# Kernel optimization log

Hardware: AMD Instinct MI355X
Metric: run time of the kernel (lower is better)

The kernel has to match this reference:

```python
import jax, jax.numpy as jnp
import numpy as np


def get_con_vecs(seq):
    # Faithful to torch: reshape (B,H,S,d) -> (B,S,H*d) (a raw reshape, as in the
    # original), right-pad along the sequence axis to length 2S with zeros, then
    # for each query position j, roll the padded sequence by (S - j).
    # Instead of a python loop of rolls over a repeated (B,S,2S,D) buffer, we
    # compute the roll as a single gather with precomputed indices.
    B, H, S, d = seq.shape
    D = H * d
    x = seq.reshape(B, S, D)
    padded = jnp.concatenate([x, jnp.zeros_like(x)], axis=1)  # (B, 2S, D)
    t = jnp.arange(2 * S)
    j = jnp.arange(S)
    # torch.roll(v, shift)[t] == v[(t - shift) mod N]; shift = S - j
    idx = (t[None, :] - (S - j[:, None])) % (2 * S)  # (S, 2S)
    new = padded[:, idx, :]  # (B, S, 2S, D)
    return new.reshape(B, H, S, 2 * S, d)


def setup_inputs() -> dict:
    key = jax.random.key(0)
    kq, kk, kv = jax.random.split(key, 3)
    B, H, S, d = 2, 8, 256, 64
    Q = jax.random.normal(kq, (B, H, S, d), dtype=jnp.float32)
    K = jax.random.normal(kk, (B, H, S, d), dtype=jnp.float32)
    V = jax.random.normal(kv, (B, H, S, d), dtype=jnp.float32)
    return {"Q": Q, "K": K, "V": V}


def reference(Q, K, V):
    # attn_type == 'con' branch of ScaledDotProductAttention.forward
    Q_c = get_con_vecs(Q)              # (B,H,S,2S,d)
    V_c = get_con_vecs(V)              # (B,H,S,2S,d)
    scores = jnp.sum(Q_c * V_c, axis=3)  # (B,H,S,d)
    attn = jax.nn.softmax(scores, axis=-1)
    context = attn * V                 # elementwise, (B,H,S,d)
    return (context, attn)
```

## Files before the change

### kernel.cpp

```cpp
#include <hip/hip_runtime.h>
#include <hip/hip_bf16.h>

#define B_ 2
#define H_ 8
#define S_ 256
#define D_ 64
#define PER_B (H_ * S_ * D_)
#define OUT_HALF (B_ * H_ * S_ * D_)
#define NR 96
#define NQ 24


__global__ __launch_bounds__(512) void k_fused(const float* __restrict__ Q,
                                               const float* __restrict__ V,
                                               float* __restrict__ out) {
    __shared__ float Gl[NR][D_];
    __shared__ float Q4[NQ][D_];
    const int lane = threadIdx.x & 63;
    const int wave = threadIdx.x >> 6;
    const int bid = blockIdx.x;
    const int m = bid & 7;
    const int h = (bid >> 3) & 7;
    const int b = bid >> 6;
    const int P0 = (m << 6) + (h << 5) + 256;

    const float* Qb = Q + b * PER_B;
    const float* Vb = V + b * PER_B;

    const int sub = lane >> 4;
    const int ec  = (lane & 15) << 2;
#pragma unroll
    for (int g = wave; g < NQ; g += 8) {
        int j = (g << 2) + sub;
        int p = (P0 + j) & 511;
        float4 acc = {0.f, 0.f, 0.f, 0.f};
        if (p < 256) {
            int off = (p >> 5) * (S_ * D_) + ((p & 31) << 3) * D_ + ec;
            const float* qp = Qb + off;
            const float* vp = Vb + off;
#pragma unroll
            for (int t0 = 0; t0 < 8; ++t0) {
                float4 q4 = *(const float4*)(qp + t0 * D_);
                float4 v4 = *(const float4*)(vp + t0 * D_);
                acc.x += q4.x * v4.x;
                acc.y += q4.y * v4.y;
                acc.z += q4.z * v4.z;
                acc.w += q4.w * v4.w;
            }
        }
        *(float4*)(&Gl[j][ec]) = acc;
    }
    __syncthreads();

#pragma unroll
    for (int q = wave; q < NQ; q += 8)
        Q4[q][lane] = Gl[4 * q][lane] + Gl[4 * q + 1][lane] +
                      Gl[4 * q + 2][lane] + Gl[4 * q + 3][lane];
    __syncthreads();

    const int k0 = wave << 2;
    float score = 0.0f;
#pragma unroll
    for (int t = 0; t < 16; ++t)
        score += Q4[wave + t][lane];

#pragma unroll
    for (int kk = 0; kk < 4; ++kk) {
        int k = k0 + kk;
        int s = (k << 3) + m;

        float mx = score;
#pragma unroll
        for (int off = 32; off > 0; off >>= 1)
            mx = fmaxf(mx, __shfl_xor(mx, off));
        float ex = __expf(score - mx);
        float sum = ex;
#pragma unroll
        for (int off = 32; off > 0; off >>= 1)
            sum += __shfl_xor(sum, off);

        float attn = ex / sum;
        int row = (b * H_ + h) * S_ + s;
        float v = V[row * D_ + lane];
        out[row * D_ + lane] = attn * v;
        out[OUT_HALF + row * D_ + lane] = attn;

        if (kk < 3)
            score += Gl[k + 64][lane] - Gl[k][lane];
    }
}

extern "C" void kernel_launch(void* const* d_in, const int* in_sizes, int n_in,
                              void* d_out, int out_size, void* d_ws, size_t ws_size,
                              hipStream_t stream) {
    const float* Q = (const float*)d_in[0];
    const float* V = (const float*)d_in[2];
    float* out = (float*)d_out;

    k_fused<<<B_ * H_ * 8, 512, 0, stream>>>(Q, V, out);
}
```

Measured before the change: 10.75 us.

## Split each block's rows in half and fold group sums via wave shuffles

Doubles the grid so each block handles 16 instead of 32 output rows, which shrinks the shared prefix window from 96 to 80 rows. The 4-row group sums are now built with cross-lane shuffles during the load phase, removing one shared-memory pass and a __syncthreads. Odd waves start from an unaligned window built from two partial rows plus 15 group sums, and the V load is hoisted ahead of the softmax reductions. The trade-off is more blocks repeating overlapping global loads.

```diff
diff --git a/kernel.cpp b/kernel.cpp
--- a/kernel.cpp
+++ b/kernel.cpp
@@ -7,8 +7,8 @@
 #define D_ 64
 #define PER_B (H_ * S_ * D_)
 #define OUT_HALF (B_ * H_ * S_ * D_)
-#define NR 96
-#define NQ 24
+#define NR 80
+#define NQ 20
 
 
 __global__ __launch_bounds__(512) void k_fused(const float* __restrict__ Q,
@@ -18,11 +18,12 @@
     __shared__ float Q4[NQ][D_];
     const int lane = threadIdx.x & 63;
     const int wave = threadIdx.x >> 6;
-    const int bid = blockIdx.x;
-    const int m = bid & 7;
-    const int h = (bid >> 3) & 7;
-    const int b = bid >> 6;
-    const int P0 = (m << 6) + (h << 5) + 256;
+    const int bid  = blockIdx.x;
+    const int half = bid & 1;
+    const int m    = (bid >> 1) & 7;
+    const int h    = (bid >> 4) & 7;
+    const int b    = bid >> 7;
+    const int P0   = (m << 6) + (h << 5) + 256 + (half << 4);
 
     const float* Qb = Q + b * PER_B;
     const float* Vb = V + b * PER_B;
@@ -49,25 +50,43 @@
             }
         }
         *(float4*)(&Gl[j][ec]) = acc;
+
+        float4 a2, a4;
+        a2.x = acc.x + __shfl_xor(acc.x, 16);
+        a2.y = acc.y + __shfl_xor(acc.y, 16);
+        a2.z = acc.z + __shfl_xor(acc.z, 16);
+        a2.w = acc.w + __shfl_xor(acc.w, 16);
+        a4.x = a2.x + __shfl_xor(a2.x, 32);
+        a4.y = a2.y + __shfl_xor(a2.y, 32);
+        a4.z = a2.z + __shfl_xor(a2.z, 32);
+        a4.w = a2.w + __shfl_xor(a2.w, 32);
+        if (sub == 0)
+            *(float4*)(&Q4[g][ec]) = a4;
     }
     __syncthreads();
 
+    const int kl0 = wave << 1;
+    float score = 0.0f;
+    if ((wave & 1) == 0) {
+        int q0 = kl0 >> 2;
 #pragma unroll
-    for (int q = wave; q < NQ; q += 8)
-        Q4[q][lane] = Gl[4 * q][lane] + Gl[4 * q + 1][lane] +
-                      Gl[4 * q + 2][lane] + Gl[4 * q + 3][lane];
-    __syncthreads();
-
-    const int k0 = wave << 2;
-    float score = 0.0f;
+        for (int t = 0; t < 16; ++t)
+            score += Q4[q0 + t][lane];
+    } else {
+        score = Gl[kl0][lane] + Gl[kl0 + 1][lane] +
+                Gl[kl0 + 62][lane] + Gl[kl0 + 63][lane];
+        int q0 = (kl0 + 2) >> 2;
 #pragma unroll
-    for (int t = 0; t < 16; ++t)
-        score += Q4[wave + t][lane];
+        for (int t = 0; t < 15; ++t)
+            score += Q4[q0 + t][lane];
+    }
 
 #pragma unroll
-    for (int kk = 0; kk < 4; ++kk) {
-        int k = k0 + kk;
-        int s = (k << 3) + m;
+    for (int kk = 0; kk < 2; ++kk) {
+        int kl = kl0 + kk;
+        int s = (((half << 4) + kl) << 3) + m;
+        int row = (b * H_ + h) * S_ + s;
+        float v = V[row * D_ + lane];
 
         float mx = score;
 #pragma unroll
@@ -80,13 +99,11 @@
             sum += __shfl_xor(sum, off);
 
         float attn = ex / sum;
-        int row = (b * H_ + h) * S_ + s;
-        float v = V[row * D_ + lane];
         out[row * D_ + lane] = attn * v;
         out[OUT_HALF + row * D_ + lane] = attn;
 
-        if (kk < 3)
-            score += Gl[k + 64][lane] - Gl[k][lane];
+        if (kk == 0)
+            score += Gl[kl + 64][lane] - Gl[kl][lane];
     }
 }
 
@@ -97,5 +114,5 @@
     const float* V = (const float*)d_in[2];
     float* out = (float*)d_out;
 
-    k_fused<<<B_ * H_ * 8, 512, 0, stream>>>(Q, V, out);
+    k_fused<<<B_ * H_ * 8 * 2, 512, 0, stream>>>(Q, V, out);
 }
```

Result: faster. 9.852 us (median of 2 runs) (-8.3%).
